# Performance work log

Hardware: AMD Instinct MI355X
Metric: run time of the kernel (lower is better)

Reference implementation:

```python
import jax, jax.numpy as jnp
import numpy as np

DM, H, B, SQ, SK = 512, 8, 8, 1024, 1024


def setup_inputs() -> dict:
    key = jax.random.key(0)
    ks = jax.random.split(key, 9)
    s = 0.02
    return {
        "Q": jax.random.normal(ks[0], (B, SQ, DM), jnp.float32),
        "K": jax.random.normal(ks[1], (B, SK, DM), jnp.float32),
        "V": jax.random.normal(ks[2], (B, SK, DM), jnp.float32),
        "mask": jax.random.randint(ks[3], (B, 1, SK), 0, 2, jnp.int32),
        "Wq": jax.random.normal(ks[4], (DM, DM), jnp.float32) * s,
        "bq": jnp.zeros((DM,), jnp.float32),
        "Wk": jax.random.normal(ks[5], (DM, DM), jnp.float32) * s,
        "bk": jnp.zeros((DM,), jnp.float32),
        "Wv": jax.random.normal(ks[6], (DM, DM), jnp.float32) * s,
        "bv": jnp.zeros((DM,), jnp.float32),
        "Wl": jax.random.normal(ks[7], (H * DM, DM), jnp.float32) * s,
        "bl": jnp.zeros((DM,), jnp.float32),
    }


def reference(Q, K, V, mask, Wq, bq, Wk, bk, Wv, bv, Wl, bl):
    # NB: the original loops h times with the SAME dense layers on full dm,
    # so all 'heads' are identical; compute once and replicate (same math).
    dm = Wq.shape[1]
    h = Wl.shape[0] // dm
    Ql = Q @ Wq + bq                                   # [B, Sq, dm]
    Kl = K @ Wk + bk                                   # [B, Sk, dm]
    Vl = V @ Wv + bv                                   # [B, Sk, dm]
    scale = jnp.sqrt(jnp.asarray(dm, jnp.float32))
    scores = jnp.einsum('bqd,bkd->bqk', Ql, Kl) / scale  # [B, Sq, Sk]
    scores = scores + mask.astype(scores.dtype) * (-1e9)  # mask [B,1,Sk] broadcasts
    att = jax.nn.softmax(scores, axis=-1)              # [B, Sq, Sk]
    head = jnp.einsum('bqk,bkd->bqd', att, Vl)         # [B, Sq, dm]
    multi = jnp.tile(head, (1, 1, h))                  # concat of h identical heads
    att_ws = jnp.broadcast_to(att[:, None], (att.shape[0], h) + att.shape[1:])
    Y = multi @ Wl + bl                                # [B, Sq, dm]
    return Y, att_ws
```

## Files before the change

### kernel.cpp

```cpp
#include <hip/hip_runtime.h>
#include <stdint.h>


typedef unsigned short u16;
typedef __attribute__((ext_vector_type(8))) short bf16x8;
typedef __attribute__((ext_vector_type(8))) unsigned short u16x8;
typedef __attribute__((ext_vector_type(4))) unsigned short u16x4;
typedef __attribute__((ext_vector_type(4))) float f32x4;

__device__ __forceinline__ u16 f2bf(float f) {
    union { float f; unsigned int u; } v; v.f = f;
    v.u += 0x7fffu + ((v.u >> 16) & 1u);
    return (u16)(v.u >> 16);
}

__device__ __forceinline__ void gld16(const u16* g, u16* l) {
#if __has_builtin(__builtin_amdgcn_global_load_lds)
    __builtin_amdgcn_global_load_lds(
        (const __attribute__((address_space(1))) void*)g,
        (__attribute__((address_space(3))) void*)l, 16, 0, 0);
#else
    *(uint4*)l = *(const uint4*)g;
#endif
}

template<int MODE>
__global__ __launch_bounds__(256, 2)
void gemm_tn(const u16* __restrict__ A, const u16* __restrict__ B, void* __restrict__ Cv,
             const float* __restrict__ bias, const int* __restrict__ mask,
             int K, int lda, int ldb, int ldc,
             long sA, long sB, long sC, long sMask, float scale)
{
    __shared__ __align__(16) u16 As[128][32];
    __shared__ __align__(16) u16 Bs[128][32];

    const int bz = blockIdx.z;
    const u16* Ab = A + (long)bz * sA;
    const u16* Bb = B + (long)bz * sB;
    const int m0 = blockIdx.x * 128;
    const int n0 = blockIdx.y * 128;
    const int t  = threadIdx.x;
    const int lane = t & 63;
    const int wm = ((t >> 6) & 1) * 64;
    const int wn = (t >> 7) * 64;

    f32x4 acc[4][4];
    #pragma unroll
    for (int i = 0; i < 4; i++)
        #pragma unroll
        for (int j = 0; j < 4; j++)
            acc[i][j] = (f32x4){0.f, 0.f, 0.f, 0.f};

    const int sr = t >> 2, sc = (t & 3) * 8;
    const int fr = lane & 15, fk = (lane >> 4) * 8;

    for (int k0 = 0; k0 < K; k0 += 32) {
        const u16* ap = Ab + (long)(m0 + sr) * lda + (k0 + sc);
        const u16* bp = Bb + (long)(n0 + sr) * ldb + (k0 + sc);
        gld16(ap,             &As[sr][sc]);
        gld16(ap + 64L * lda, &As[sr + 64][sc]);
        gld16(bp,             &Bs[sr][sc]);
        gld16(bp + 64L * ldb, &Bs[sr + 64][sc]);
        __syncthreads();

        bf16x8 af[4], bfv[4];
        #pragma unroll
        for (int i = 0; i < 4; i++) af[i]  = *(const bf16x8*)&As[wm + i*16 + fr][fk];
        #pragma unroll
        for (int j = 0; j < 4; j++) bfv[j] = *(const bf16x8*)&Bs[wn + j*16 + fr][fk];
        #pragma unroll
        for (int i = 0; i < 4; i++)
            #pragma unroll
            for (int j = 0; j < 4; j++)
                acc[i][j] = __builtin_amdgcn_mfma_f32_16x16x32_bf16(af[i], bfv[j], acc[i][j], 0, 0, 0);
        __syncthreads();
    }

    const int cl = lane & 15, rl = (lane >> 4) * 4;
    if (MODE == 1) {
        u16* C = (u16*)Cv + (long)bz * sC;
        #pragma unroll
        for (int i = 0; i < 4; i++)
            #pragma unroll
            for (int r = 0; r < 4; r++) {
                long row = m0 + wm + i * 16 + rl + r;
                #pragma unroll
                for (int j = 0; j < 4; j++) {
                    long col = n0 + wn + j * 16 + cl;
                    C[col * ldc + row] = f2bf(acc[i][j][r]);
                }
            }
    } else {
        float badd[4];
        #pragma unroll
        for (int j = 0; j < 4; j++) {
            int col = n0 + wn + j * 16 + cl;
            float v = bias ? bias[col] : 0.f;
            if (MODE == 2 && mask) v += (float)mask[(long)bz * sMask + col] * (-1e9f);
            badd[j] = v;
        }
        if (MODE == 0) {
            u16* C = (u16*)Cv + (long)bz * sC;
            #pragma unroll
            for (int i = 0; i < 4; i++)
                #pragma unroll
                for (int r = 0; r < 4; r++) {
                    u16* crow = C + (long)(m0 + wm + i * 16 + rl + r) * ldc;
                    #pragma unroll
                    for (int j = 0; j < 4; j++)
                        crow[n0 + wn + j * 16 + cl] = f2bf(acc[i][j][r] + badd[j]);
                }
        } else {
            float* C = (float*)Cv + (long)bz * sC;
            #pragma unroll
            for (int i = 0; i < 4; i++)
                #pragma unroll
                for (int r = 0; r < 4; r++) {
                    float* crow = C + (long)(m0 + wm + i * 16 + rl + r) * ldc;
                    #pragma unroll
                    for (int j = 0; j < 4; j++)
                        crow[n0 + wn + j * 16 + cl] = acc[i][j][r] * scale + badd[j];
                }
        }
    }
}

__global__ __launch_bounds__(256)
void prep_qkv(const float* __restrict__ Q, const float* __restrict__ K,
              const float* __restrict__ V, u16* __restrict__ Qb,
              u16* __restrict__ Kb, u16* __restrict__ Vb)
{
    long id = (long)blockIdx.x * 256 + threadIdx.x;
    int seg = (int)(id >> 19);
    long e = (id & 524287L) * 8;
    const float* s = seg == 0 ? Q : (seg == 1 ? K : V);
    u16* d = seg == 0 ? Qb : (seg == 1 ? Kb : Vb);
    float4 lo = *(const float4*)(s + e);
    float4 hi = *(const float4*)(s + e + 4);
    u16x8 r;
    r[0]=f2bf(lo.x); r[1]=f2bf(lo.y); r[2]=f2bf(lo.z); r[3]=f2bf(lo.w);
    r[4]=f2bf(hi.x); r[5]=f2bf(hi.y); r[6]=f2bf(hi.z); r[7]=f2bf(hi.w);
    *(u16x8*)(d + e) = r;
}

__global__ __launch_bounds__(256)
void prep_w(const float* __restrict__ Wq, const float* __restrict__ Wk,
            const float* __restrict__ Wv, const float* __restrict__ Wl,
            u16* __restrict__ Wqt, u16* __restrict__ Wkt,
            u16* __restrict__ Wvt, u16* __restrict__ Wst)
{
    long id = (long)blockIdx.x * 256 + threadIdx.x;
    int seg = (int)(id >> 18);
    long j = id & 262143L;
    int n = (int)(j & 511), k = (int)(j >> 9);
    if (seg < 3) {
        const float* W = seg == 0 ? Wq : (seg == 1 ? Wk : Wv);
        u16* Wt = seg == 0 ? Wqt : (seg == 1 ? Wkt : Wvt);
        Wt[(long)n * 512 + k] = f2bf(W[(long)k * 512 + n]);
    } else {
        float s = 0.f;
        #pragma unroll
        for (int h = 0; h < 8; h++) s += Wl[((long)h * 512 + k) * 512 + n];
        Wst[(long)n * 512 + k] = f2bf(s);
    }
}

__global__ __launch_bounds__(256)
void softmax_rep(float* __restrict__ att, u16* __restrict__ attb)
{
    const int q = blockIdx.x, b = blockIdx.y;
    const int t = threadIdx.x;
    float* row0 = att + ((long)b * 8 * 1024 + q) * 1024;

    float4 xv = *(const float4*)(row0 + t * 4);
    float x[4] = {xv.x, xv.y, xv.z, xv.w};

    float m = fmaxf(fmaxf(x[0], x[1]), fmaxf(x[2], x[3]));
    #pragma unroll
    for (int o = 32; o > 0; o >>= 1) m = fmaxf(m, __shfl_xor(m, o));
    __shared__ float red[4];
    const int w = t >> 6;
    if ((t & 63) == 0) red[w] = m;
    __syncthreads();
    m = fmaxf(fmaxf(red[0], red[1]), fmaxf(red[2], red[3]));
    __syncthreads();

    float e[4], s = 0.f;
    #pragma unroll
    for (int i = 0; i < 4; i++) { e[i] = __expf(x[i] - m); s += e[i]; }
    #pragma unroll
    for (int o = 32; o > 0; o >>= 1) s += __shfl_xor(s, o);
    if ((t & 63) == 0) red[w] = s;
    __syncthreads();
    s = red[0] + red[1] + red[2] + red[3];
    float inv = 1.f / s;

    float a0 = e[0]*inv, a1 = e[1]*inv, a2 = e[2]*inv, a3 = e[3]*inv;
    float4 ov = make_float4(a0, a1, a2, a3);
    #pragma unroll
    for (int h = 0; h < 8; h++)
        *(float4*)(att + (((long)b * 8 + h) * 1024 + q) * 1024 + t * 4) = ov;
    u16x4 bo; bo[0]=f2bf(a0); bo[1]=f2bf(a1); bo[2]=f2bf(a2); bo[3]=f2bf(a3);
    *(u16x4*)(attb + ((long)b * 1024 + q) * 1024 + t * 4) = bo;
}

extern "C" void kernel_launch(void* const* d_in, const int* in_sizes, int n_in,
                              void* d_out, int out_size, void* d_ws, size_t ws_size,
                              hipStream_t stream)
{
    (void)in_sizes; (void)n_in; (void)out_size; (void)ws_size;

    const float* Q    = (const float*)d_in[0];
    const float* Kin  = (const float*)d_in[1];
    const float* V    = (const float*)d_in[2];
    const int*   mask = (const int*)d_in[3];
    const float* Wq   = (const float*)d_in[4];
    const float* bq   = (const float*)d_in[5];
    const float* Wk   = (const float*)d_in[6];
    const float* bk   = (const float*)d_in[7];
    const float* Wv   = (const float*)d_in[8];
    const float* bv   = (const float*)d_in[9];
    const float* Wl   = (const float*)d_in[10];
    const float* bl   = (const float*)d_in[11];

    float* out  = (float*)d_out;
    float* Yout = out;
    float* att  = out + 4194304L;

    u16* w    = (u16*)d_ws;
    u16* Qb   = w;
    u16* Kb   = Qb + 4194304L;
    u16* Vb   = Kb + 4194304L;
    u16* Wqt  = Vb + 4194304L;
    u16* Wkt  = Wqt + 262144L;
    u16* Wvt  = Wkt + 262144L;
    u16* Wst  = Wvt + 262144L;
    u16* Qlb  = Wst + 262144L;
    u16* Klb  = Qlb + 4194304L;
    u16* Vt   = Klb + 4194304L;
    u16* attb = Vt + 4194304L;
    u16* Hd   = attb + 8388608L;

    const long sQ  = 524288L;
    const long sAt = 1048576L;
    const long BATT = 8L * 1048576L;
    const float isc = 0.04419417382415922f;

    prep_qkv<<<dim3(6144), dim3(256), 0, stream>>>(Q, Kin, V, Qb, Kb, Vb);
    prep_w<<<dim3(4096), dim3(256), 0, stream>>>(Wq, Wk, Wv, Wl, Wqt, Wkt, Wvt, Wst);

    gemm_tn<0><<<dim3(8, 4, 8), dim3(256), 0, stream>>>(
        Qb, Wqt, Qlb, bq, nullptr, 512, 512, 512, 512, sQ, 0L, sQ, 0L, 1.f);
    gemm_tn<0><<<dim3(8, 4, 8), dim3(256), 0, stream>>>(
        Kb, Wkt, Klb, bk, nullptr, 512, 512, 512, 512, sQ, 0L, sQ, 0L, 1.f);
    gemm_tn<1><<<dim3(8, 4, 8), dim3(256), 0, stream>>>(
        Vb, Wvt, Vt, bv, nullptr, 512, 512, 512, 1024, sQ, 0L, sQ, 0L, 1.f);

    gemm_tn<2><<<dim3(8, 8, 8), dim3(256), 0, stream>>>(
        Qlb, Klb, att, nullptr, mask, 512, 512, 512, 1024,
        sQ, sQ, BATT, 1024L, isc);

    softmax_rep<<<dim3(1024, 8), dim3(256), 0, stream>>>(att, attb);

    gemm_tn<0><<<dim3(8, 4, 8), dim3(256), 0, stream>>>(
        attb, Vt, Hd, nullptr, nullptr, 1024, 1024, 1024, 512,
        sAt, sQ, sQ, 0L, 1.f);

    gemm_tn<2><<<dim3(8, 4, 8), dim3(256), 0, stream>>>(
        Hd, Wst, Yout, bl, nullptr, 512, 512, 512, 512, sQ, 0L, sQ, 0L, 1.f);
}
```

Measured before the change: 464.5 us.

## Fold output projection into V weights, fuse QKV GEMMs, store scores as bf16

Folds the summed output projection into the value weights (Wv·Wsum), so the final projection GEMM disappears and att@V writes Y directly. The bias term becomes bv·Wsum. The Q/K/V projections now run in one batched launch, and the folded-weight GEMM shares a launch with the input conversion. Scores are written as bf16 to a scratch buffer instead of fp32 into the att output, which cuts score traffic. This adds bf16 rounding of the scores before softmax and a different rounding order from the folded weight product.

Result: no change. 469.5 us (+1.1%).

```diff
diff --git a/kernel.cpp b/kernel.cpp
--- a/kernel.cpp
+++ b/kernel.cpp
@@ -12,6 +12,10 @@
     union { float f; unsigned int u; } v; v.f = f;
     v.u += 0x7fffu + ((v.u >> 16) & 1u);
     return (u16)(v.u >> 16);
+}
+__device__ __forceinline__ float bf2f(u16 u) {
+    union { unsigned int u; float f; } v; v.u = (unsigned int)u << 16;
+    return v.f;
 }
 
 __device__ __forceinline__ void gld16(const u16* g, u16* l) {
@@ -24,33 +28,14 @@
 #endif
 }
 
-template<int MODE>
-__global__ __launch_bounds__(256, 2)
-void gemm_tn(const u16* __restrict__ A, const u16* __restrict__ B, void* __restrict__ Cv,
-             const float* __restrict__ bias, const int* __restrict__ mask,
-             int K, int lda, int ldb, int ldc,
-             long sA, long sB, long sC, long sMask, float scale)
-{
-    __shared__ __align__(16) u16 As[128][32];
-    __shared__ __align__(16) u16 Bs[128][32];
-
-    const int bz = blockIdx.z;
-    const u16* Ab = A + (long)bz * sA;
-    const u16* Bb = B + (long)bz * sB;
-    const int m0 = blockIdx.x * 128;
-    const int n0 = blockIdx.y * 128;
-    const int t  = threadIdx.x;
+__device__ __forceinline__ void gemm_core(
+    const u16* __restrict__ Ab, const u16* __restrict__ Bb,
+    int K, int lda, int ldb, int m0, int n0, int t,
+    u16 (*As)[32], u16 (*Bs)[32], f32x4 acc[4][4])
+{
     const int lane = t & 63;
     const int wm = ((t >> 6) & 1) * 64;
     const int wn = (t >> 7) * 64;
-
-    f32x4 acc[4][4];
-    #pragma unroll
-    for (int i = 0; i < 4; i++)
-        #pragma unroll
-        for (int j = 0; j < 4; j++)
-            acc[i][j] = (f32x4){0.f, 0.f, 0.f, 0.f};
-
     const int sr = t >> 2, sc = (t & 3) * 8;
     const int fr = lane & 15, fk = (lane >> 4) * 8;
 
@@ -75,88 +60,154 @@
                 acc[i][j] = __builtin_amdgcn_mfma_f32_16x16x32_bf16(af[i], bfv[j], acc[i][j], 0, 0, 0);
         __syncthreads();
     }
-
+}
+
+__device__ __forceinline__ void gemm_epilogue(
+    int mode, void* Cv, const float* bias, const int* maskp,
+    float scale, int ldc, int m0, int n0, int t, f32x4 acc[4][4])
+{
+    const int lane = t & 63;
+    const int wm = ((t >> 6) & 1) * 64;
+    const int wn = (t >> 7) * 64;
     const int cl = lane & 15, rl = (lane >> 4) * 4;
-    if (MODE == 1) {
-        u16* C = (u16*)Cv + (long)bz * sC;
+
+    float badd[4];
+    #pragma unroll
+    for (int j = 0; j < 4; j++) {
+        int col = n0 + wn + j * 16 + cl;
+        float v = bias ? bias[col] : 0.f;
+        if (maskp) v += (float)maskp[col] * (-1e9f);
+        badd[j] = v;
+    }
+
+    if (mode == 1) {
+        u16* C = (u16*)Cv;
         #pragma unroll
         for (int i = 0; i < 4; i++)
             #pragma unroll
             for (int r = 0; r < 4; r++) {
                 long row = m0 + wm + i * 16 + rl + r;
                 #pragma unroll
-                for (int j = 0; j < 4; j++) {
-                    long col = n0 + wn + j * 16 + cl;
-                    C[col * ldc + row] = f2bf(acc[i][j][r]);
-                }
+                for (int j = 0; j < 4; j++)
+                    C[(long)(n0 + wn + j * 16 + cl) * ldc + row] =
+                        f2bf(acc[i][j][r] * scale + badd[j]);
+            }
+    } else if (mode == 2) {
+        float* C = (float*)Cv;
+        #pragma unroll
+        for (int i = 0; i < 4; i++)
+            #pragma unroll
+            for (int r = 0; r < 4; r++) {
+                float* crow = C + (long)(m0 + wm + i * 16 + rl + r) * ldc;
+                #pragma unroll
+                for (int j = 0; j < 4; j++)
+                    crow[n0 + wn + j * 16 + cl] = acc[i][j][r] * scale + badd[j];
             }
     } else {
-        float badd[4];
-        #pragma unroll
-        for (int j = 0; j < 4; j++) {
-            int col = n0 + wn + j * 16 + cl;
-            float v = bias ? bias[col] : 0.f;
-            if (MODE == 2 && mask) v += (float)mask[(long)bz * sMask + col] * (-1e9f);
-            badd[j] = v;
-        }
-        if (MODE == 0) {
-            u16* C = (u16*)Cv + (long)bz * sC;
+        u16* C = (u16*)Cv;
+        #pragma unroll
+        for (int i = 0; i < 4; i++)
             #pragma unroll
-            for (int i = 0; i < 4; i++)
+            for (int r = 0; r < 4; r++) {
+                u16* crow = C + (long)(m0 + wm + i * 16 + rl + r) * ldc;
                 #pragma unroll
-                for (int r = 0; r < 4; r++) {
-                    u16* crow = C + (long)(m0 + wm + i * 16 + rl + r) * ldc;
-                    #pragma unroll
-                    for (int j = 0; j < 4; j++)
-                        crow[n0 + wn + j * 16 + cl] = f2bf(acc[i][j][r] + badd[j]);
-                }
-        } else {
-            float* C = (float*)Cv + (long)bz * sC;
-            #pragma unroll
-            for (int i = 0; i < 4; i++)
-                #pragma unroll
-                for (int r = 0; r < 4; r++) {
-                    float* crow = C + (long)(m0 + wm + i * 16 + rl + r) * ldc;
-                    #pragma unroll
-                    for (int j = 0; j < 4; j++)
-                        crow[n0 + wn + j * 16 + cl] = acc[i][j][r] * scale + badd[j];
-                }
-        }
-    }
-}
-
-__global__ __launch_bounds__(256)
-void prep_qkv(const float* __restrict__ Q, const float* __restrict__ K,
-              const float* __restrict__ V, u16* __restrict__ Qb,
-              u16* __restrict__ Kb, u16* __restrict__ Vb)
-{
-    long id = (long)blockIdx.x * 256 + threadIdx.x;
-    int seg = (int)(id >> 19);
-    long e = (id & 524287L) * 8;
-    const float* s = seg == 0 ? Q : (seg == 1 ? K : V);
-    u16* d = seg == 0 ? Qb : (seg == 1 ? Kb : Vb);
-    float4 lo = *(const float4*)(s + e);
-    float4 hi = *(const float4*)(s + e + 4);
-    u16x8 r;
-    r[0]=f2bf(lo.x); r[1]=f2bf(lo.y); r[2]=f2bf(lo.z); r[3]=f2bf(lo.w);
-    r[4]=f2bf(hi.x); r[5]=f2bf(hi.y); r[6]=f2bf(hi.z); r[7]=f2bf(hi.w);
-    *(u16x8*)(d + e) = r;
+                for (int j = 0; j < 4; j++)
+                    crow[n0 + wn + j * 16 + cl] = f2bf(acc[i][j][r] * scale + badd[j]);
+            }
+    }
+}
+
+__global__ __launch_bounds__(256, 2)
+void gemm_tn(const u16* __restrict__ A, const u16* __restrict__ B, void* __restrict__ Cv,
+             const float* __restrict__ bias, const int* __restrict__ mask,
+             int K, int lda, int ldb, int ldc,
+             long sA, long sB, long sC, long sMask, float scale, int mode)
+{
+    __shared__ __align__(16) u16 As[128][32];
+    __shared__ __align__(16) u16 Bs[128][32];
+    const int bz = blockIdx.z;
+    const int m0 = blockIdx.x * 128, n0 = blockIdx.y * 128;
+    const int t = threadIdx.x;
+
+    f32x4 acc[4][4];
+    #pragma unroll
+    for (int i = 0; i < 4; i++)
+        #pragma unroll
+        for (int j = 0; j < 4; j++) acc[i][j] = (f32x4){0.f, 0.f, 0.f, 0.f};
+
+    gemm_core(A + (long)bz * sA, B + (long)bz * sB, K, lda, ldb, m0, n0, t, As, Bs, acc);
+
+    void* Cb = (mode == 2) ? (void*)((float*)Cv + (long)bz * sC)
+                           : (void*)((u16*)Cv + (long)bz * sC);
+    const int* maskp = mask ? mask + (long)bz * sMask : nullptr;
+    gemm_epilogue(mode, Cb, bias, maskp, scale, ldc, m0, n0, t, acc);
+}
+
+__global__ __launch_bounds__(256, 2)
+void gemm_qkvv(const u16* __restrict__ Qb, const u16* __restrict__ Kb,
+               const u16* __restrict__ Vb, const u16* __restrict__ Wqt,
+               const u16* __restrict__ Wkt, const u16* __restrict__ Wct,
+               u16* __restrict__ Qlb, u16* __restrict__ Klb, u16* __restrict__ Vwt,
+               const float* __restrict__ bq, const float* __restrict__ bk,
+               const float* __restrict__ bvs)
+{
+    __shared__ __align__(16) u16 As[128][32];
+    __shared__ __align__(16) u16 Bs[128][32];
+    const int z = blockIdx.z, seg = z >> 3, b = z & 7;
+    const int m0 = blockIdx.x * 128, n0 = blockIdx.y * 128;
+    const int t = threadIdx.x;
+    const long sQ = 524288L;
+
+    const u16* A; const u16* B; u16* C; const float* bias; int ldc, mode;
+    if (seg == 0)      { A = Qb + b * sQ; B = Wqt; C = Qlb + b * sQ; bias = bq;  ldc = 512;  mode = 0; }
+    else if (seg == 1) { A = Kb + b * sQ; B = Wkt; C = Klb + b * sQ; bias = bk;  ldc = 512;  mode = 0; }
+    else               { A = Vb + b * sQ; B = Wct; C = Vwt + b * sQ; bias = bvs; ldc = 1024; mode = 1; }
+
+    f32x4 acc[4][4];
+    #pragma unroll
+    for (int i = 0; i < 4; i++)
+        #pragma unroll
+        for (int j = 0; j < 4; j++) acc[i][j] = (f32x4){0.f, 0.f, 0.f, 0.f};
+
+    gemm_core(A, B, 512, 512, 512, m0, n0, t, As, Bs, acc);
+    gemm_epilogue(mode, C, bias, nullptr, 1.f, ldc, m0, n0, t, acc);
 }
 
 __global__ __launch_bounds__(256)
 void prep_w(const float* __restrict__ Wq, const float* __restrict__ Wk,
             const float* __restrict__ Wv, const float* __restrict__ Wl,
+            const float* __restrict__ bv,
             u16* __restrict__ Wqt, u16* __restrict__ Wkt,
-            u16* __restrict__ Wvt, u16* __restrict__ Wst)
-{
-    long id = (long)blockIdx.x * 256 + threadIdx.x;
+            u16* __restrict__ Wvb, u16* __restrict__ Wst, float* __restrict__ bvs)
+{
+    const int bx = blockIdx.x;
+    if (bx >= 4096) {
+        int n = (bx - 4096) * 256 + threadIdx.x;
+        if (n < 512) {
+            float acc = 0.f;
+            for (int k = 0; k < 512; k++) {
+                float bvk = bv[k];
+                if (bvk != 0.f) {
+                    float s = 0.f;
+                    #pragma unroll
+                    for (int h = 0; h < 8; h++) s += Wl[((long)h * 512 + k) * 512 + n];
+                    acc += bvk * s;
+                }
+            }
+            bvs[n] = acc;
+        }
+        return;
+    }
+    long id = (long)bx * 256 + threadIdx.x;
     int seg = (int)(id >> 18);
     long j = id & 262143L;
     int n = (int)(j & 511), k = (int)(j >> 9);
-    if (seg < 3) {
-        const float* W = seg == 0 ? Wq : (seg == 1 ? Wk : Wv);
-        u16* Wt = seg == 0 ? Wqt : (seg == 1 ? Wkt : Wvt);
-        Wt[(long)n * 512 + k] = f2bf(W[(long)k * 512 + n]);
+    if (seg == 0) {
+        Wqt[(long)n * 512 + k] = f2bf(Wq[(long)k * 512 + n]);
+    } else if (seg == 1) {
+        Wkt[(long)n * 512 + k] = f2bf(Wk[(long)k * 512 + n]);
+    } else if (seg == 2) {
+        Wvb[j] = f2bf(Wv[j]);
     } else {
         float s = 0.f;
         #pragma unroll
@@ -165,15 +216,52 @@
     }
 }
 
+__global__ __launch_bounds__(256, 2)
+void prep_qkv_wct(const float* __restrict__ Q, const float* __restrict__ K,
+                  const float* __restrict__ V, u16* __restrict__ Qb,
+                  u16* __restrict__ Kb, u16* __restrict__ Vb,
+                  const u16* __restrict__ Wvb, const u16* __restrict__ Wst,
+                  u16* __restrict__ Wct)
+{
+    __shared__ __align__(16) u16 As[128][32];
+    __shared__ __align__(16) u16 Bs[128][32];
+    const int bx = blockIdx.x;
+    if (bx < 6144) {
+        long id = (long)bx * 256 + threadIdx.x;
+        int seg = (int)(id >> 19);
+        long e = (id & 524287L) * 8;
+        const float* s = seg == 0 ? Q : (seg == 1 ? K : V);
+        u16* d = seg == 0 ? Qb : (seg == 1 ? Kb : Vb);
+        float4 lo = *(const float4*)(s + e);
+        float4 hi = *(const float4*)(s + e + 4);
+        u16x8 r;
+        r[0]=f2bf(lo.x); r[1]=f2bf(lo.y); r[2]=f2bf(lo.z); r[3]=f2bf(lo.w);
+        r[4]=f2bf(hi.x); r[5]=f2bf(hi.y); r[6]=f2bf(hi.z); r[7]=f2bf(hi.w);
+        *(u16x8*)(d + e) = r;
+        return;
+    }
+    const int bid = bx - 6144;
+    const int m0 = (bid & 3) * 128, n0 = (bid >> 2) * 128;
+    const int t = threadIdx.x;
+    f32x4 acc[4][4];
+    #pragma unroll
+    for (int i = 0; i < 4; i++)
+        #pragma unroll
+        for (int j = 0; j < 4; j++) acc[i][j] = (f32x4){0.f, 0.f, 0.f, 0.f};
+    gemm_core(Wvb, Wst, 512, 512, 512, m0, n0, t, As, Bs, acc);
+    gemm_epilogue(1, Wct, nullptr, nullptr, 1.f, 512, m0, n0, t, acc);
+}
+
 __global__ __launch_bounds__(256)
-void softmax_rep(float* __restrict__ att, u16* __restrict__ attb)
+void softmax_rep(const u16* __restrict__ Sb, float* __restrict__ att,
+                 u16* __restrict__ attb)
 {
     const int q = blockIdx.x, b = blockIdx.y;
     const int t = threadIdx.x;
-    float* row0 = att + ((long)b * 8 * 1024 + q) * 1024;
-
-    float4 xv = *(const float4*)(row0 + t * 4);
-    float x[4] = {xv.x, xv.y, xv.z, xv.w};
+    const u16* row = Sb + ((long)b * 1024 + q) * 1024;
+
+    u16x4 xv = *(const u16x4*)(row + t * 4);
+    float x[4] = { bf2f(xv[0]), bf2f(xv[1]), bf2f(xv[2]), bf2f(xv[3]) };
 
     float m = fmaxf(fmaxf(x[0], x[1]), fmaxf(x[2], x[3]));
     #pragma unroll
@@ -227,45 +315,42 @@
     float* Yout = out;
     float* att  = out + 4194304L;
 
-    u16* w    = (u16*)d_ws;
-    u16* Qb   = w;
-    u16* Kb   = Qb + 4194304L;
-    u16* Vb   = Kb + 4194304L;
-    u16* Wqt  = Vb + 4194304L;
-    u16* Wkt  = Wqt + 262144L;
-    u16* Wvt  = Wkt + 262144L;
-    u16* Wst  = Wvt + 262144L;
-    u16* Qlb  = Wst + 262144L;
-    u16* Klb  = Qlb + 4194304L;
-    u16* Vt   = Klb + 4194304L;
-    u16* attb = Vt + 4194304L;
-    u16* Hd   = attb + 8388608L;
+    u16*   w    = (u16*)d_ws;
+    float* bvs  = (float*)w;
+    u16*   Qb   = w + 1024;
+    u16*   Kb   = Qb + 4194304L;
+    u16*   Vb   = Kb + 4194304L;
+    u16*   Wqt  = Vb + 4194304L;
+    u16*   Wkt  = Wqt + 262144L;
+    u16*   Wvb  = Wkt + 262144L;
+    u16*   Wst  = Wvb + 262144L;
+    u16*   Wct  = Wst + 262144L;
+    u16*   Qlb  = Wct + 262144L;
+    u16*   Klb  = Qlb + 4194304L;
+    u16*   Vwt  = Klb + 4194304L;
+    u16*   Sb   = Vwt + 4194304L;
+    u16*   attb = Sb + 8388608L;
 
     const long sQ  = 524288L;
     const long sAt = 1048576L;
-    const long BATT = 8L * 1048576L;
     const float isc = 0.04419417382415922f;
 
-    prep_qkv<<<dim3(6144), dim3(256), 0, stream>>>(Q, Kin, V, Qb, Kb, Vb);
-    prep_w<<<dim3(4096), dim3(256), 0, stream>>>(Wq, Wk, Wv, Wl, Wqt, Wkt, Wvt, Wst);
-
-    gemm_tn<0><<<dim3(8, 4, 8), dim3(256), 0, stream>>>(
-        Qb, Wqt, Qlb, bq, nullptr, 512, 512, 512, 512, sQ, 0L, sQ, 0L, 1.f);
-    gemm_tn<0><<<dim3(8, 4, 8), dim3(256), 0, stream>>>(
-        Kb, Wkt, Klb, bk, nullptr, 512, 512, 512, 512, sQ, 0L, sQ, 0L, 1.f);
-    gemm_tn<1><<<dim3(8, 4, 8), dim3(256), 0, stream>>>(
-        Vb, Wvt, Vt, bv, nullptr, 512, 512, 512, 1024, sQ, 0L, sQ, 0L, 1.f);
-
-    gemm_tn<2><<<dim3(8, 8, 8), dim3(256), 0, stream>>>(
-        Qlb, Klb, att, nullptr, mask, 512, 512, 512, 1024,
-        sQ, sQ, BATT, 1024L, isc);
-
-    softmax_rep<<<dim3(1024, 8), dim3(256), 0, stream>>>(att, attb);
-
-    gemm_tn<0><<<dim3(8, 4, 8), dim3(256), 0, stream>>>(
-        attb, Vt, Hd, nullptr, nullptr, 1024, 1024, 1024, 512,
-        sAt, sQ, sQ, 0L, 1.f);
-
-    gemm_tn<2><<<dim3(8, 4, 8), dim3(256), 0, stream>>>(
-        Hd, Wst, Yout, bl, nullptr, 512, 512, 512, 512, sQ, 0L, sQ, 0L, 1.f);
-}
+    prep_w<<<dim3(4098), dim3(256), 0, stream>>>(Wq, Wk, Wv, Wl, bv,
+                                                 Wqt, Wkt, Wvb, Wst, bvs);
+
+    prep_qkv_wct<<<dim3(6160), dim3(256), 0, stream>>>(Q, Kin, V, Qb, Kb, Vb,
+                                                       Wvb, Wst, Wct);
+
+    gemm_qkvv<<<dim3(8, 4, 24), dim3(256), 0, stream>>>(
+        Qb, Kb, Vb, Wqt, Wkt, Wct, Qlb, Klb, Vwt, bq, bk, bvs);
+
+    gemm_tn<<<dim3(8, 8, 8), dim3(256), 0, stream>>>(
+        Qlb, Klb, Sb, nullptr, mask, 512, 512, 512, 1024,
+        sQ, sQ, sAt, 1024L, isc, 0);
+
+    softmax_rep<<<dim3(1024, 8), dim3(256), 0, stream>>>(Sb, att, attb);
+
+    gemm_tn<<<dim3(8, 4, 8), dim3(256), 0, stream>>>(
+        attb, Vwt, Yout, bl, nullptr, 1024, 1024, 1024, 512,
+        sAt, sQ, sQ, 0L, 1.f, 2);
+}
```
